# Performance work log

Measured on AMD Instinct MI355X. Metric: run time of the kernel, lower is better.

The kernel has to match this reference:

```python
import jax, jax.numpy as jnp
import numpy as np

B, T, I, H, O = 512, 1024, 15, 64, 11

def setup_inputs() -> dict:
    key = jax.random.key(0)
    ks = jax.random.split(key, 7)
    s_ih = 1.0 / np.sqrt(H)
    return {
        "x": jax.random.normal(ks[0], (B, T, I), dtype=jnp.float32),
        # torch nn.RNN params: weight_ih_l0 [H,I], weight_hh_l0 [H,H], biases [H]
        "W_ih": jax.random.uniform(ks[1], (H, I), jnp.float32, -s_ih, s_ih),
        "b_ih": jax.random.uniform(ks[2], (H,), jnp.float32, -s_ih, s_ih),
        "W_hh": jax.random.uniform(ks[3], (H, H), jnp.float32, -s_ih, s_ih),
        "b_hh": jax.random.uniform(ks[4], (H,), jnp.float32, -s_ih, s_ih),
        # decoder Linear(64, 11)
        "W_dec": jax.random.uniform(ks[5], (O, H), jnp.float32, -s_ih, s_ih),
        "b_dec": jax.random.uniform(ks[6], (O,), jnp.float32, -s_ih, s_ih),
    }

def reference(x, W_ih, b_ih, W_hh, b_hh, W_dec, b_dec):
    # Precompute input projection for all timesteps: [T, B, H]
    xproj = jnp.einsum("bti,hi->tbh", x, W_ih) + b_ih + b_hh
    h0 = jnp.zeros((x.shape[0], W_hh.shape[0]), dtype=x.dtype)

    def step(h, xp_t):
        h_new = jax.nn.relu(xp_t + h @ W_hh.T)  # [B, H]
        return h_new, h_new

    h_last, hs = jax.lax.scan(step, h0, xproj)  # hs: [T, B, H]
    out_seq = jnp.transpose(hs, (1, 0, 2))       # [B, T, H]
    out = jax.nn.relu(jnp.einsum("bth,oh->bto", out_seq, W_dec) + b_dec)
    h = h_last[None]  # [1, B, H] matching torch num_layers dim
    return (out, h)
```

## Files before the change

### kernel.cpp

```cpp
#include <hip/hip_runtime.h>
#include <hip/hip_fp16.h>
#include <stdint.h>

#define BB 512
#define TT 1024
#define II 15
#define HH 64
#define OO 11
#define NC (TT / 64)

typedef __fp16 half2v __attribute__((ext_vector_type(2)));
typedef float floatx4 __attribute__((ext_vector_type(4)));
typedef int int4v __attribute__((ext_vector_type(4)));

union PK { int i; half2v h; float f; };

__device__ __forceinline__ half2v i2h2(int v) { PK u; u.i = v; return u.h; }
__device__ __forceinline__ int h22i(half2v v) { PK u; u.h = v; return u.i; }

__device__ __forceinline__ float FDOT2(half2v a, half2v b, float c) {
    return __builtin_amdgcn_fdot2(a, b, c, false);
}

__device__ __forceinline__ float lane_xor1(float v) {
    PK u; u.f = v;
    u.i = __builtin_amdgcn_mov_dpp(u.i, 0xB1, 0xF, 0xF, false);
    return u.f;
}

__device__ __forceinline__ float lane_xor2(float v) {
    PK u; u.f = v;
    u.i = __builtin_amdgcn_mov_dpp(u.i, 0x4E, 0xF, 0xF, false);
    return u.f;
}

__device__ __forceinline__ void block_sync() {
    asm volatile("s_waitcnt lgkmcnt(0)" ::: "memory");
    __builtin_amdgcn_s_barrier();
}

__global__ __launch_bounds__(256) void rnn_fused(
    const float* __restrict__ x, const float* __restrict__ W_ih,
    const float* __restrict__ b_ih, const float* __restrict__ W_hh,
    const float* __restrict__ b_hh, const float* __restrict__ W_dec,
    const float* __restrict__ b_dec, float* __restrict__ out,
    float* __restrict__ h_last)
{
    __shared__ __align__(16) int xpack[2][64 * 8];
    __shared__ __align__(16) float xsbuf[2][2][64 * 64];
    __shared__ __align__(16) _Float16 hring[2][128][HH];
    const int tid  = threadIdx.x;
    const int lane = tid & 63;
    const int wid  = tid >> 6;
    const int w = wid & 1;
    const int b = blockIdx.x * 2 + w;
    const float* xb = x + (size_t)b * TT * II;

    if (wid < 2) {
        half2v whh[32];
#pragma unroll
        for (int p = 0; p < 32; ++p)
            whh[p] = __builtin_amdgcn_cvt_pkrtz(W_hh[lane * HH + 2 * p],
                                                W_hh[lane * HH + 2 * p + 1]);

        hring[w][127][lane] = (_Float16)0.0f;

        block_sync();

        float h = 0.0f;
        int hpk = 0;

        for (int c = 0; c < NC; ++c) {
            const float* xsp = &xsbuf[w][c & 1][0];
            for (int to = 0; to < 64; to += 8) {
#pragma unroll
                for (int u = 0; u < 8; ++u) {
                    const int ts = to + u;
                    const int t = c * 64 + ts;

                    const int4v* hb4 =
                        (const int4v*)&hring[w][(t + 127) & 127][0];
                    int4v hb[6];
#pragma unroll
                    for (int q = 0; q < 6; ++q) hb[q] = hb4[q + 2];
                    const float xsv = xsp[ts * 64 + lane];

                    float a0, a1, a2, a3, a4, a5, a6, a7;
                    a0 = FDOT2(i2h2(__builtin_amdgcn_readlane(hpk, 0)),  whh[0], 0.0f);
                    a1 = FDOT2(i2h2(__builtin_amdgcn_readlane(hpk, 2)),  whh[1], 0.0f);
                    a2 = FDOT2(i2h2(__builtin_amdgcn_readlane(hpk, 4)),  whh[2], 0.0f);
                    a3 = FDOT2(i2h2(__builtin_amdgcn_readlane(hpk, 6)),  whh[3], 0.0f);
                    a4 = FDOT2(i2h2(__builtin_amdgcn_readlane(hpk, 8)),  whh[4], 0.0f);
                    a5 = FDOT2(i2h2(__builtin_amdgcn_readlane(hpk, 10)), whh[5], 0.0f);
                    a6 = FDOT2(i2h2(__builtin_amdgcn_readlane(hpk, 12)), whh[6], 0.0f);
                    a7 = FDOT2(i2h2(__builtin_amdgcn_readlane(hpk, 14)), whh[7], 0.0f);

#pragma unroll
                    for (int q = 0; q < 6; ++q) {
                        const int base = 8 + 4 * q;
                        if ((q & 1) == 0) {
                            a0 = FDOT2(i2h2(hb[q].x), whh[base + 0], a0);
                            a1 = FDOT2(i2h2(hb[q].y), whh[base + 1], a1);
                            a2 = FDOT2(i2h2(hb[q].z), whh[base + 2], a2);
                            a3 = FDOT2(i2h2(hb[q].w), whh[base + 3], a3);
                        } else {
                            a4 = FDOT2(i2h2(hb[q].x), whh[base + 0], a4);
                            a5 = FDOT2(i2h2(hb[q].y), whh[base + 1], a5);
                            a6 = FDOT2(i2h2(hb[q].z), whh[base + 2], a6);
                            a7 = FDOT2(i2h2(hb[q].w), whh[base + 3], a7);
                        }
                    }
                    const float s = ((a0 + a1) + (a2 + a3)) +
                                    ((a4 + a5) + (a6 + a7));
                    h = fmaxf(s + xsv, 0.0f);
                    hring[w][t & 127][lane] = (_Float16)h;

                    hpk = h22i(__builtin_amdgcn_cvt_pkrtz(h, lane_xor1(h)));
                }
            }
            block_sync();
        }
        h_last[b * HH + lane] = h;
    } else {
        half2v wx[8];
#pragma unroll
        for (int j = 0; j < 7; ++j)
            wx[j] = __builtin_amdgcn_cvt_pkrtz(W_ih[lane * II + 2 * j],
                                               W_ih[lane * II + 2 * j + 1]);
        wx[7] = __builtin_amdgcn_cvt_pkrtz(W_ih[lane * II + 14],
                                           b_ih[lane] + b_hh[lane]);

        const int od = lane >> 2;
        const int oc = (od < OO) ? od : 0;
        const int ks = lane & 3;
        half2v wdec[8];
#pragma unroll
        for (int p = 0; p < 8; ++p)
            wdec[p] = __builtin_amdgcn_cvt_pkrtz(
                W_dec[oc * HH + (ks * 8 + p) * 2],
                W_dec[oc * HH + (ks * 8 + p) * 2 + 1]);
        const float bd = b_dec[oc];
        const bool dostore = (ks == 0) && (od < OO);
        float* outb = out + (size_t)b * TT * OO + od;

        auto stage_xs = [&](int chunk) __attribute__((always_inline)) {
            const float* xc = xb + (size_t)(chunk * 64 + lane) * II;
            float cf[II];
#pragma unroll
            for (int i = 0; i < II; ++i) cf[i] = xc[i];
            int4v p0, p1;
            p0.x = h22i(__builtin_amdgcn_cvt_pkrtz(cf[0], cf[1]));
            p0.y = h22i(__builtin_amdgcn_cvt_pkrtz(cf[2], cf[3]));
            p0.z = h22i(__builtin_amdgcn_cvt_pkrtz(cf[4], cf[5]));
            p0.w = h22i(__builtin_amdgcn_cvt_pkrtz(cf[6], cf[7]));
            p1.x = h22i(__builtin_amdgcn_cvt_pkrtz(cf[8], cf[9]));
            p1.y = h22i(__builtin_amdgcn_cvt_pkrtz(cf[10], cf[11]));
            p1.z = h22i(__builtin_amdgcn_cvt_pkrtz(cf[12], cf[13]));
            p1.w = h22i(__builtin_amdgcn_cvt_pkrtz(cf[14], 1.0f));
            *(int4v*)&xpack[w][lane * 8] = p0;
            *(int4v*)&xpack[w][lane * 8 + 4] = p1;

            const int4v* xp4 = (const int4v*)&xpack[w][0];
            float* xsd = &xsbuf[w][chunk & 1][0];
#pragma unroll 4
            for (int ts = 0; ts < 64; ++ts) {
                const int4v xv0 = xp4[2 * ts];
                const int4v xv1 = xp4[2 * ts + 1];
                float t0 = FDOT2(i2h2(xv0.x), wx[0], 0.0f);
                float t1 = FDOT2(i2h2(xv0.y), wx[1], 0.0f);
                float t2 = FDOT2(i2h2(xv0.z), wx[2], 0.0f);
                float t3 = FDOT2(i2h2(xv0.w), wx[3], 0.0f);
                float t4 = FDOT2(i2h2(xv1.x), wx[4], 0.0f);
                float t5 = FDOT2(i2h2(xv1.y), wx[5], 0.0f);
                float t6 = FDOT2(i2h2(xv1.z), wx[6], 0.0f);
                float t7 = FDOT2(i2h2(xv1.w), wx[7], 0.0f);
                xsd[ts * 64 + lane] = ((t0 + t1) + (t2 + t3)) +
                                      ((t4 + t5) + (t6 + t7));
            }
        };

        auto decode_chunk = [&](int c) __attribute__((always_inline)) {
#pragma unroll 4
            for (int lt = 0; lt < 64; ++lt) {
                const int t = c * 64 + lt;
                const char* row = (const char*)&hring[w][t & 127][0];
                const int4v d0 = *(const int4v*)(row + ks * 32);
                const int4v d1 = *(const int4v*)(row + ks * 32 + 16);
                float dacc = FDOT2(i2h2(d0.x), wdec[0], 0.0f);
                dacc = FDOT2(i2h2(d0.y), wdec[1], dacc);
                dacc = FDOT2(i2h2(d0.z), wdec[2], dacc);
                dacc = FDOT2(i2h2(d0.w), wdec[3], dacc);
                dacc = FDOT2(i2h2(d1.x), wdec[4], dacc);
                dacc = FDOT2(i2h2(d1.y), wdec[5], dacc);
                dacc = FDOT2(i2h2(d1.z), wdec[6], dacc);
                dacc = FDOT2(i2h2(d1.w), wdec[7], dacc);
                dacc += lane_xor1(dacc);
                dacc += lane_xor2(dacc);
                if (dostore)
                    outb[(size_t)t * OO] = fmaxf(dacc + bd, 0.0f);
            }
        };

        stage_xs(0);
        block_sync();

        for (int c = 0; c < NC; ++c) {
            if (c + 1 < NC) stage_xs(c + 1);
            if (c >= 1) decode_chunk(c - 1);
            block_sync();
        }
        decode_chunk(NC - 1);
    }
}

extern "C" void kernel_launch(void* const* d_in, const int* in_sizes, int n_in,
                              void* d_out, int out_size, void* d_ws, size_t ws_size,
                              hipStream_t stream) {
    const float* x     = (const float*)d_in[0];
    const float* W_ih  = (const float*)d_in[1];
    const float* b_ih  = (const float*)d_in[2];
    const float* W_hh  = (const float*)d_in[3];
    const float* b_hh  = (const float*)d_in[4];
    const float* W_dec = (const float*)d_in[5];
    const float* b_dec = (const float*)d_in[6];

    float* out    = (float*)d_out;
    float* h_last = out + (size_t)BB * TT * OO;

    rnn_fused<<<BB / 2, 256, 0, stream>>>(x, W_ih, b_ih, W_hh, b_hh,
                                          W_dec, b_dec, out, h_last);
}
```

Baseline: 246.7 us.

## Compute recurrent matvec with MFMA 16x16x32 instead of packed dot2

Replaces the per-lane fdot2 chain over W_hh (readlane broadcasts plus LDS reads of the previous hidden state) with eight MFMA 16x16x32 f16 ops. The A operand is built by ds_bpermute broadcasting the packed hidden state, and one output row of each MFMA is selected per lane. This targets the serial per-step latency of the recurrence, at the cost of wasting most MFMA rows and adding MFMA and bpermute latency onto the critical path.

Measured after the change: 251.3 us. Within noise of the previous version (+1.9%).

```diff
diff --git a/kernel.cpp b/kernel.cpp
--- a/kernel.cpp
+++ b/kernel.cpp
@@ -10,10 +10,12 @@
 #define NC (TT / 64)
 
 typedef __fp16 half2v __attribute__((ext_vector_type(2)));
+typedef _Float16 half8 __attribute__((ext_vector_type(8)));
 typedef float floatx4 __attribute__((ext_vector_type(4)));
 typedef int int4v __attribute__((ext_vector_type(4)));
 
 union PK { int i; half2v h; float f; };
+union AU { int4v i; half8 h; };
 
 __device__ __forceinline__ half2v i2h2(int v) { PK u; u.i = v; return u.h; }
 __device__ __forceinline__ int h22i(half2v v) { PK u; u.h = v; return u.i; }
@@ -57,13 +59,27 @@
     const float* xb = x + (size_t)b * TT * II;
 
     if (wid < 2) {
-        half2v whh[32];
-#pragma unroll
-        for (int p = 0; p < 32; ++p)
-            whh[p] = __builtin_amdgcn_cvt_pkrtz(W_hh[lane * HH + 2 * p],
-                                                W_hh[lane * HH + 2 * p + 1]);
-
-        hring[w][127][lane] = (_Float16)0.0f;
+        const int nl = lane & 15;
+        const int kq = lane >> 4;
+        half8 bf[4][2];
+#pragma unroll
+        for (int g = 0; g < 4; ++g)
+#pragma unroll
+            for (int s = 0; s < 2; ++s)
+#pragma unroll
+                for (int j = 0; j < 8; ++j)
+                    bf[g][s][j] = (_Float16)W_hh[(16 * g + nl) * HH +
+                                                 32 * s + 8 * kq + j];
+
+        int bpidx[8];
+#pragma unroll
+        for (int jj = 0; jj < 4; ++jj) {
+            bpidx[jj]     = kq * 32 + 8 * jj;
+            bpidx[jj + 4] = bpidx[jj] + 128;
+        }
+        const bool bsel4 = (lane & 16) != 0;
+        const bool bsel5 = (lane & 32) != 0;
+        const floatx4 zc = {0.0f, 0.0f, 0.0f, 0.0f};
 
         block_sync();
 
@@ -77,42 +93,39 @@
                 for (int u = 0; u < 8; ++u) {
                     const int ts = to + u;
                     const int t = c * 64 + ts;
-
-                    const int4v* hb4 =
-                        (const int4v*)&hring[w][(t + 127) & 127][0];
-                    int4v hb[6];
-#pragma unroll
-                    for (int q = 0; q < 6; ++q) hb[q] = hb4[q + 2];
                     const float xsv = xsp[ts * 64 + lane];
 
-                    float a0, a1, a2, a3, a4, a5, a6, a7;
-                    a0 = FDOT2(i2h2(__builtin_amdgcn_readlane(hpk, 0)),  whh[0], 0.0f);
-                    a1 = FDOT2(i2h2(__builtin_amdgcn_readlane(hpk, 2)),  whh[1], 0.0f);
-                    a2 = FDOT2(i2h2(__builtin_amdgcn_readlane(hpk, 4)),  whh[2], 0.0f);
-                    a3 = FDOT2(i2h2(__builtin_amdgcn_readlane(hpk, 6)),  whh[3], 0.0f);
-                    a4 = FDOT2(i2h2(__builtin_amdgcn_readlane(hpk, 8)),  whh[4], 0.0f);
-                    a5 = FDOT2(i2h2(__builtin_amdgcn_readlane(hpk, 10)), whh[5], 0.0f);
-                    a6 = FDOT2(i2h2(__builtin_amdgcn_readlane(hpk, 12)), whh[6], 0.0f);
-                    a7 = FDOT2(i2h2(__builtin_amdgcn_readlane(hpk, 14)), whh[7], 0.0f);
-
-#pragma unroll
-                    for (int q = 0; q < 6; ++q) {
-                        const int base = 8 + 4 * q;
-                        if ((q & 1) == 0) {
-                            a0 = FDOT2(i2h2(hb[q].x), whh[base + 0], a0);
-                            a1 = FDOT2(i2h2(hb[q].y), whh[base + 1], a1);
-                            a2 = FDOT2(i2h2(hb[q].z), whh[base + 2], a2);
-                            a3 = FDOT2(i2h2(hb[q].w), whh[base + 3], a3);
-                        } else {
-                            a4 = FDOT2(i2h2(hb[q].x), whh[base + 0], a4);
-                            a5 = FDOT2(i2h2(hb[q].y), whh[base + 1], a5);
-                            a6 = FDOT2(i2h2(hb[q].z), whh[base + 2], a6);
-                            a7 = FDOT2(i2h2(hb[q].w), whh[base + 3], a7);
-                        }
-                    }
-                    const float s = ((a0 + a1) + (a2 + a3)) +
-                                    ((a4 + a5) + (a6 + a7));
-                    h = fmaxf(s + xsv, 0.0f);
+                    const int r0 = __builtin_amdgcn_ds_bpermute(bpidx[0], hpk);
+                    const int r1 = __builtin_amdgcn_ds_bpermute(bpidx[1], hpk);
+                    const int r2 = __builtin_amdgcn_ds_bpermute(bpidx[2], hpk);
+                    const int r3 = __builtin_amdgcn_ds_bpermute(bpidx[3], hpk);
+                    const int r4 = __builtin_amdgcn_ds_bpermute(bpidx[4], hpk);
+                    const int r5 = __builtin_amdgcn_ds_bpermute(bpidx[5], hpk);
+                    const int r6 = __builtin_amdgcn_ds_bpermute(bpidx[6], hpk);
+                    const int r7 = __builtin_amdgcn_ds_bpermute(bpidx[7], hpk);
+                    AU au0; au0.i = (int4v){r0, r1, r2, r3};
+                    AU au1; au1.i = (int4v){r4, r5, r6, r7};
+                    const half8 a0 = au0.h;
+                    const half8 a1 = au1.h;
+
+                    floatx4 c0 = __builtin_amdgcn_mfma_f32_16x16x32_f16(a0, bf[0][0], zc, 0, 0, 0);
+                    floatx4 d0 = __builtin_amdgcn_mfma_f32_16x16x32_f16(a1, bf[0][1], zc, 0, 0, 0);
+                    floatx4 c1 = __builtin_amdgcn_mfma_f32_16x16x32_f16(a0, bf[1][0], zc, 0, 0, 0);
+                    floatx4 d1 = __builtin_amdgcn_mfma_f32_16x16x32_f16(a1, bf[1][1], zc, 0, 0, 0);
+                    floatx4 c2 = __builtin_amdgcn_mfma_f32_16x16x32_f16(a0, bf[2][0], zc, 0, 0, 0);
+                    floatx4 d2 = __builtin_amdgcn_mfma_f32_16x16x32_f16(a1, bf[2][1], zc, 0, 0, 0);
+                    floatx4 c3 = __builtin_amdgcn_mfma_f32_16x16x32_f16(a0, bf[3][0], zc, 0, 0, 0);
+                    floatx4 d3 = __builtin_amdgcn_mfma_f32_16x16x32_f16(a1, bf[3][1], zc, 0, 0, 0);
+
+                    const float v0 = c0[0] + d0[0];
+                    const float v1 = c1[0] + d1[0];
+                    const float v2 = c2[0] + d2[0];
+                    const float v3 = c3[0] + d3[0];
+                    const float r01 = bsel4 ? v1 : v0;
+                    const float r23 = bsel4 ? v3 : v2;
+                    const float hpre = bsel5 ? r23 : r01;
+
+                    h = fmaxf(hpre + xsv, 0.0f);
                     hring[w][t & 127][lane] = (_Float16)h;
 
                     hpk = h22i(__builtin_amdgcn_cvt_pkrtz(h, lane_xor1(h)));
```
